# Kernel optimization log

Hardware: AMD Instinct MI355X
Metric: run time of the kernel (lower is better)

The kernel has to match this reference:

```python
import jax, jax.numpy as jnp
import numpy as np

D = 256
H = 8
DH = D // H
EPS = 1e-3  # keras LayerNormalization default epsilon


def sinusoidal_pe(length, dim):
    pos = jnp.arange(length, dtype=jnp.float32)[:, None]            # [L,1]
    i = jnp.arange(0, dim, 2, dtype=jnp.float32)[None, :]           # [1,D/2]
    angle = pos / jnp.power(10000.0, i / dim)                        # [L,D/2]
    pe = jnp.zeros((length, dim), dtype=jnp.float32)
    pe = pe.at[:, 0::2].set(jnp.sin(angle))
    pe = pe.at[:, 1::2].set(jnp.cos(angle))
    return pe


def rel_shift(x):
    # x: [B,H,L,L] -> Transformer-XL relative shift
    B, h, L1, L2 = x.shape
    x = jnp.pad(x, ((0, 0), (0, 0), (0, 0), (1, 0)))                 # [B,H,L,L+1]
    x = x.reshape(B, h, L2 + 1, L1)[:, :, 1:, :]                     # drop first row
    return x.reshape(B, h, L1, L2)


def setup_inputs() -> dict:
    key = jax.random.key(0)
    ks = jax.random.split(key, 16)
    s = 0.02
    inp = {
        "x": jax.random.normal(ks[0], (4, 2048, D), dtype=jnp.float32),
        "gamma": jnp.ones((D,), dtype=jnp.float32),
        "beta": jnp.zeros((D,), dtype=jnp.float32),
        "Wq": jax.random.normal(ks[1], (D, D), dtype=jnp.float32) * s,
        "bq": jnp.zeros((D,), dtype=jnp.float32),
        "Wk": jax.random.normal(ks[2], (D, D), dtype=jnp.float32) * s,
        "bk": jnp.zeros((D,), dtype=jnp.float32),
        "Wv": jax.random.normal(ks[3], (D, D), dtype=jnp.float32) * s,
        "bv": jnp.zeros((D,), dtype=jnp.float32),
        "Wp": jax.random.normal(ks[4], (D, D), dtype=jnp.float32) * s,  # pos proj, no bias
        "u_bias": jax.random.normal(ks[5], (H, DH), dtype=jnp.float32) * s,
        "v_bias": jax.random.normal(ks[6], (H, DH), dtype=jnp.float32) * s,
        "Wo": jax.random.normal(ks[7], (D, D), dtype=jnp.float32) * s,
        "bo": jnp.zeros((D,), dtype=jnp.float32),
    }
    return inp


def reference(x, gamma, beta, Wq, bq, Wk, bk, Wv, bv, Wp, u_bias, v_bias, Wo, bo):
    B, L, _ = x.shape
    # pre-LN (keras LayerNormalization over last axis)
    mu = jnp.mean(x, axis=-1, keepdims=True)
    var = jnp.mean(jnp.square(x - mu), axis=-1, keepdims=True)
    xn = (x - mu) * jax.lax.rsqrt(var + EPS) * gamma + beta

    pe = sinusoidal_pe(L, D)                                          # [L,D] (tiled over batch implicitly)

    q = (xn @ Wq + bq).reshape(B, L, H, DH)                           # [B,L,H,dh]
    k = (xn @ Wk + bk).reshape(B, L, H, DH)
    v = (xn @ Wv + bv).reshape(B, L, H, DH)
    p = (pe @ Wp).reshape(L, H, DH)                                   # [L,H,dh]

    # content and position scores (Transformer-XL biases u, v)
    content = jnp.einsum("bqhd,bkhd->bhqk", q + u_bias[None, None], k)
    pos = jnp.einsum("bqhd,khd->bhqk", q + v_bias[None, None], p)
    pos = rel_shift(pos)
    score = (content + pos) / jnp.sqrt(jnp.float32(D))

    attn = jax.nn.softmax(score, axis=-1)                             # dropout inactive (inference)
    ctx = jnp.einsum("bhqk,bkhd->bqhd", attn, v).reshape(B, L, D)
    out = ctx @ Wo + bo                                               # final dropout inactive
    return out
```

## Files before the change

kernel.cpp:

```cpp
#include <hip/hip_runtime.h>
#include <hip/hip_bf16.h>
#include <math.h>

#define L_SEQ 2048
#define NB 4
#define DMODEL 256
#define NH 8
#define DHEAD 32
#define NROW (NB*L_SEQ)

typedef __attribute__((ext_vector_type(8))) short short8;
typedef __attribute__((ext_vector_type(4))) float f32x4;

__device__ __forceinline__ float bf2f(short v) {
    union { unsigned u; float f; } x; x.u = ((unsigned)(unsigned short)v) << 16; return x.f;
}
__device__ __forceinline__ short f2bf(float f) {
    union { float f; unsigned u; } x; x.f = f;
    unsigned r = x.u + 0x7fff + ((x.u >> 16) & 1);
    return (short)(r >> 16);
}
__device__ __forceinline__ short8 zero8() {
    short8 z;
    #pragma unroll
    for (int i = 0; i < 8; ++i) z[i] = 0;
    return z;
}

__global__ __launch_bounds__(256)
void prep_kernel(const float* __restrict__ x, const float* __restrict__ gamma,
                 const float* __restrict__ beta, short* __restrict__ xnb,
                 short* __restrict__ peb,
                 const float* __restrict__ W0, const float* __restrict__ W1,
                 const float* __restrict__ W2, const float* __restrict__ W3,
                 const float* __restrict__ W4, short* __restrict__ WT,
                 short* __restrict__ pext) {
    const int bid = blockIdx.x;
    __shared__ float s[64][65];
    if (bid < 2048) {
        int lane = threadIdx.x & 63;
        int row  = bid*4 + (threadIdx.x >> 6);
        const float4 a = *(const float4*)(x + (size_t)row*DMODEL + lane*4);
        float sm  = a.x+a.y+a.z+a.w;
        float s2 = a.x*a.x+a.y*a.y+a.z*a.z+a.w*a.w;
        #pragma unroll
        for (int o = 32; o; o >>= 1) { sm += __shfl_xor(sm,o); s2 += __shfl_xor(s2,o); }
        float mu  = sm * (1.f/DMODEL);
        float var = s2 * (1.f/DMODEL) - mu*mu;
        float rst = rsqrtf(var + 1e-3f);
        const float4 g  = *(const float4*)(gamma + lane*4);
        const float4 bt = *(const float4*)(beta  + lane*4);
        short4 o;
        o.x = f2bf((a.x-mu)*rst*g.x + bt.x);
        o.y = f2bf((a.y-mu)*rst*g.y + bt.y);
        o.z = f2bf((a.z-mu)*rst*g.z + bt.z);
        o.w = f2bf((a.w-mu)*rst*g.w + bt.w);
        *(short4*)(xnb + (size_t)row*DMODEL + lane*4) = o;
    } else if (bid < 3072) {
        int idx = (bid-2048)*256 + threadIdx.x;
        int l = idx >> 7, m = idx & 127;
        double ang = (double)l * exp((double)m * (-9.210340371976184/128.0));
        unsigned sv = (unsigned)(unsigned short)f2bf((float)sin(ang));
        unsigned cv = (unsigned)(unsigned short)f2bf((float)cos(ang));
        *(unsigned*)(peb + l*DMODEL + 2*m) = sv | (cv << 16);
    } else if (bid < 3152) {
        const int r  = bid - 3072;
        const int z  = r >> 4, rr = r & 15;
        const float* W = (z==0)?W0:(z==1)?W1:(z==2)?W2:(z==3)?W3:W4;
        short* O = WT + (size_t)z*65536;
        const int k0 = (rr >> 2)*64, n0 = (rr & 3)*64;
        const int c = threadIdx.x & 63, r4 = threadIdx.x >> 6;
        #pragma unroll
        for (int i = 0; i < 16; ++i) {
            int rw = r4 + 4*i;
            s[c][rw] = W[(size_t)(k0+rw)*256 + n0 + c];
        }
        __syncthreads();
        #pragma unroll
        for (int i = 0; i < 16; ++i) {
            int rn = r4 + 4*i;
            O[(size_t)(n0+rn)*256 + k0 + c] = f2bf(s[rn][c]);
        }
    } else {
        if (threadIdx.x < 64) {
            short4 z4 = {0,0,0,0};
            *(short4*)(pext + (size_t)L_SEQ*DMODEL + threadIdx.x*4) = z4;
        }
    }
}

__global__ __launch_bounds__(256, 2)
void projmm_kernel(const short* __restrict__ xnb, const short* __restrict__ peb,
                   const short* __restrict__ WT,
                   const float* __restrict__ bq, const float* __restrict__ bk,
                   const float* __restrict__ bv,
                   short* __restrict__ q, short* __restrict__ kb,
                   short* __restrict__ vT, short* __restrict__ pext) {
    const int bid = blockIdx.x;
    int z, rb;
    if (bid < 384) { z = bid >> 7; rb = bid & 127; }
    else           { z = 3;        rb = bid - 384; }
    const short* A = (z == 3) ? peb : xnb;
    const short* W = WT + (size_t)z*65536;
    const int t = threadIdx.x;
    const int w = t >> 6, l = t & 63, lc = l & 15, lg = l >> 4;
    const int m0 = rb*64 + 16*w;

    short8 afr[8];
    #pragma unroll
    for (int ks = 0; ks < 8; ++ks)
        afr[ks] = *(const short8*)(A + (size_t)(m0+lc)*256 + ks*32 + lg*8);

    const f32x4 zf = {0.f,0.f,0.f,0.f};
    f32x4 acc[16];
    #pragma unroll
    for (int ct = 0; ct < 16; ++ct) acc[ct] = zf;

    #pragma unroll
    for (int ct = 0; ct < 16; ++ct) {
        #pragma unroll
        for (int ks = 0; ks < 8; ++ks) {
            const short8 bfr = *(const short8*)(W + (size_t)(ct*16+lc)*256 + ks*32 + lg*8);
            acc[ct] = __builtin_amdgcn_mfma_f32_16x16x32_bf16(afr[ks], bfr, acc[ct], 0, 0, 0);
        }
    }

    if (z == 2) {
        const int bb = m0 >> 11;
        const int l0 = (m0 & 2047) + 4*lg;
        #pragma unroll
        for (int ct = 0; ct < 16; ++ct) {
            const int cc = ct*16 + lc;
            const float bias = bv[cc];
            const int hh = cc >> 5, dd = cc & 31;
            short4 o;
            o.x = f2bf(acc[ct][0] + bias);
            o.y = f2bf(acc[ct][1] + bias);
            o.z = f2bf(acc[ct][2] + bias);
            o.w = f2bf(acc[ct][3] + bias);
            *(short4*)(vT + ((size_t)((bb*NH + hh)*DHEAD + dd))*L_SEQ + l0) = o;
        }
    } else if (z == 3) {
        #pragma unroll
        for (int ct = 0; ct < 16; ++ct) {
            const int cc = ct*16 + lc;
            #pragma unroll
            for (int r = 0; r < 4; ++r) {
                const int rr = m0 + 4*lg + r;
                const short v = f2bf(acc[ct][r]);
                pext[(size_t)rr*DMODEL + cc] = v;
                pext[(size_t)(rr + L_SEQ + 1)*DMODEL + cc] = v;
            }
        }
    } else {
        #pragma unroll
        for (int ct = 0; ct < 16; ++ct) {
            const int cc = ct*16 + lc;
            const float bias = (z == 0) ? bq[cc] : bk[cc];
            #pragma unroll
            for (int r = 0; r < 4; ++r) {
                const size_t idx = (size_t)(m0 + 4*lg + r)*DMODEL + cc;
                const short v = f2bf(acc[ct][r] + bias);
                if (z == 0) q[idx] = v;
                else        kb[idx] = v;
            }
        }
    }
}

__global__ __launch_bounds__(256, 2)
void outmm_kernel(const short* __restrict__ ctxb, const short* __restrict__ WTo,
                  const float* __restrict__ bo, float* __restrict__ out) {
    const int rb = blockIdx.x;
    const int t = threadIdx.x;
    const int w = t >> 6, l = t & 63, lc = l & 15, lg = l >> 4;
    const int m0 = rb*64 + 16*w;

    short8 afr[8];
    #pragma unroll
    for (int ks = 0; ks < 8; ++ks)
        afr[ks] = *(const short8*)(ctxb + (size_t)(m0+lc)*256 + ks*32 + lg*8);

    const f32x4 zf = {0.f,0.f,0.f,0.f};
    f32x4 acc[16];
    #pragma unroll
    for (int ct = 0; ct < 16; ++ct) acc[ct] = zf;

    #pragma unroll
    for (int ct = 0; ct < 16; ++ct) {
        #pragma unroll
        for (int ks = 0; ks < 8; ++ks) {
            const short8 bfr = *(const short8*)(WTo + (size_t)(ct*16+lc)*256 + ks*32 + lg*8);
            acc[ct] = __builtin_amdgcn_mfma_f32_16x16x32_bf16(afr[ks], bfr, acc[ct], 0, 0, 0);
        }
    }

    #pragma unroll
    for (int ct = 0; ct < 16; ++ct) {
        const int cc = ct*16 + lc;
        const float bias = bo[cc];
        #pragma unroll
        for (int r = 0; r < 4; ++r)
            out[(size_t)(m0 + 4*lg + r)*DMODEL + cc] = acc[ct][r] + bias;
    }
}

__global__ __launch_bounds__(256)
void attn_mfma_kernel(const short* __restrict__ qg, const short* __restrict__ kb,
                      const short* __restrict__ pext, const short* __restrict__ vT,
                      const float* __restrict__ ub, const float* __restrict__ vb,
                      short* __restrict__ ctxb) {
    const int i0  = blockIdx.x;
    const int xcd = i0 & 7, idx = i0 >> 3;
    const int h   = xcd;
    const int b   = idx >> 4;
    const int w   = threadIdx.x >> 6;
    const int q0  = (idx & 15) * 128 + 32 * w;
    const int l   = threadIdx.x & 63;
    const int lc  = l & 15;
    const int lg  = l >> 4;

    __shared__ float    sT[4][2][17][84];
    __shared__ unsigned sPk[4][2][2][16][32];

    const float KSC = 0.0625f * 1.44269504088896340736f;

    short8 aqu[2], aqv[2], aqv_sh[2];
    #pragma unroll
    for (int g = 0; g < 2; ++g) {
        const int r1 = q0 + 16*g + lc;
        const short8 qraw = *(const short8*)(qg + ((size_t)(b*L_SEQ + r1))*DMODEL + h*DHEAD + lg*8);
        short8 qraw_sh = zero8();
        if (r1 + 1 < L_SEQ)
            qraw_sh = *(const short8*)(qg + ((size_t)(b*L_SEQ + r1 + 1))*DMODEL + h*DHEAD + lg*8);
        #pragma unroll
        for (int j = 0; j < 8; ++j) {
            const float u_ = ub[h*DHEAD + lg*8 + j];
            const float v_ = vb[h*DHEAD + lg*8 + j];
            const float f  = bf2f(qraw[j]);
            aqu[g][j]    = f2bf((f + u_) * KSC);
            aqv[g][j]    = f2bf((f + v_) * KSC);
            aqv_sh[g][j] = f2bf((bf2f(qraw_sh[j]) + v_) * KSC);
        }
    }

    float m_r[2] = {-3.0e38f, -3.0e38f}, l_r[2] = {0.f, 0.f};
    f32x4 acc[2][2];
    #pragma unroll
    for (int g = 0; g < 2; ++g)
        #pragma unroll
        for (int dt = 0; dt < 2; ++dt)
            acc[g][dt] = (f32x4){0.f,0.f,0.f,0.f};
    const f32x4 zf = {0.f, 0.f, 0.f, 0.f};

    const short* kfetch = kb + ((size_t)(b*L_SEQ) + lc)*DMODEL + h*DHEAD + lg*8;
    const short* pcur   = pext + ((size_t)(L_SEQ - 32 - q0 + lc))*DMODEL + h*DHEAD + lg*8;
    const short* vcur   = vT + ((size_t)((b*NH + h)*DHEAD + lc))*L_SEQ + lg*8;

    short8 kfrag[4], pfrag[6], vfrag[2][2];
    #pragma unroll
    for (int ct = 0; ct < 4; ++ct)
        kfrag[ct] = *(const short8*)(kfetch + (size_t)ct*16*DMODEL);
    #pragma unroll
    for (int s = 0; s < 6; ++s)
        pfrag[s] = *(const short8*)(pcur + (size_t)s*16*DMODEL);
    kfetch += (size_t)64*DMODEL;

    const int colc = 4*lg + 15 - lc;
    const float* gb0[2] = { &sT[w][0][lc][colc],   &sT[w][1][lc][colc]   };
    const float* gb1[2] = { &sT[w][0][lc+1][colc], &sT[w][1][lc+1][colc] };
    const int swkey = lc & 7;

    for (int k0 = 0; k0 < L_SEQ; k0 += 64) {
        const int diff = k0 - q0;
        const int tbuf = (k0 >> 6) & 1;

        f32x4 cts[2][4];
        #pragma unroll
        for (int ct = 0; ct < 4; ++ct) {
            cts[0][ct] = __builtin_amdgcn_mfma_f32_16x16x32_bf16(kfrag[ct], aqu[0], zf, 0, 0, 0);
            cts[1][ct] = __builtin_amdgcn_mfma_f32_16x16x32_bf16(kfrag[ct], aqu[1], zf, 0, 0, 0);
        }

        #pragma unroll
        for (int g = 0; g < 2; ++g) {
            const int cthr = 17 - diff + 16*g;
            const int sb = 1 - g;
            if (cthr > 78) {
                #pragma unroll
                for (int cc = 0; cc < 5; ++cc) {
                    f32x4 tt = __builtin_amdgcn_mfma_f32_16x16x32_bf16(pfrag[cc+sb], aqv[g], zf, 0, 0, 0);
                    *(f32x4*)&sT[w][g][lc][16*cc + 4*lg] = tt;
                }
            } else if (cthr <= 0) {
                #pragma unroll
                for (int cc = 0; cc < 5; ++cc) {
                    f32x4 tt = __builtin_amdgcn_mfma_f32_16x16x32_bf16(pfrag[cc+sb], aqv_sh[g], zf, 0, 0, 0);
                    *(f32x4*)&sT[w][g][lc][16*cc + 4*lg] = tt;
                }
            } else {
                #pragma unroll
                for (int cc = 0; cc < 5; ++cc) {
                    f32x4 tt = __builtin_amdgcn_mfma_f32_16x16x32_bf16(pfrag[cc+sb], aqv[g], zf, 0, 0, 0);
                    *(f32x4*)&sT[w][g][lc][16*cc + 4*lg] = tt;
                    f32x4 tt2 = __builtin_amdgcn_mfma_f32_16x16x32_bf16(pfrag[cc+sb], aqv_sh[g], zf, 0, 0, 0);
                    if (lc == 15) *(f32x4*)&sT[w][g][16][16*cc + 4*lg] = tt2;
                }
            }
        }

        pfrag[0] = pfrag[4];
        pfrag[1] = pfrag[5];
        if (k0 + 64 < L_SEQ) {
            #pragma unroll
            for (int ct = 0; ct < 4; ++ct)
                kfrag[ct] = *(const short8*)(kfetch + (size_t)ct*16*DMODEL);
            #pragma unroll
            for (int s = 2; s < 6; ++s)
                pfrag[s] = *(const short8*)(pcur + (size_t)(64 + 16*s)*DMODEL);
        }
        kfetch += (size_t)64*DMODEL;
        pcur   += (size_t)64*DMODEL;

        asm volatile("s_waitcnt lgkmcnt(0)" ::: "memory");

        if (k0) {
            #pragma unroll
            for (int kc = 0; kc < 2; ++kc) {
                const int idx2 = ((4*kc + lg) ^ swkey) << 2;
                const short8 bp0 = *(const short8*)&sPk[w][0][tbuf ^ 1][lc][idx2];
                const short8 bp1 = *(const short8*)&sPk[w][1][tbuf ^ 1][lc][idx2];
                acc[0][0] = __builtin_amdgcn_mfma_f32_16x16x32_bf16(vfrag[0][kc], bp0, acc[0][0], 0, 0, 0);
                acc[0][1] = __builtin_amdgcn_mfma_f32_16x16x32_bf16(vfrag[1][kc], bp0, acc[0][1], 0, 0, 0);
                acc[1][0] = __builtin_amdgcn_mfma_f32_16x16x32_bf16(vfrag[0][kc], bp1, acc[1][0], 0, 0, 0);
                acc[1][1] = __builtin_amdgcn_mfma_f32_16x16x32_bf16(vfrag[1][kc], bp1, acc[1][1], 0, 0, 0);
            }
        }
        #pragma unroll
        for (int dt = 0; dt < 2; ++dt)
            #pragma unroll
            for (int kc = 0; kc < 2; ++kc)
                vfrag[dt][kc] = *(const short8*)(vcur + (size_t)dt*16*L_SEQ + kc*32);
        vcur += 64;

        float sc[2][4][4];
        float pmax[2];
        #pragma unroll
        for (int g = 0; g < 2; ++g) {
            const int cthr = 17 - diff + 16*g;
            if (cthr > 78 || cthr <= 0) {
                #pragma unroll
                for (int ct = 0; ct < 4; ++ct)
                    #pragma unroll
                    for (int r = 0; r < 4; ++r)
                        sc[g][ct][r] = cts[g][ct][r] + gb0[g][16*ct + r];
            } else {
                #pragma unroll
                for (int ct = 0; ct < 4; ++ct)
                    #pragma unroll
                    for (int r = 0; r < 4; ++r) {
                        const bool up = (16*ct + colc + r) >= cthr;
                        sc[g][ct][r] = cts[g][ct][r] + (up ? gb1[g] : gb0[g])[16*ct + r];
                    }
            }
            pmax[g] = sc[g][0][0];
            #pragma unroll
            for (int ct = 0; ct < 4; ++ct)
                #pragma unroll
                for (int r = 0; r < 4; ++r) pmax[g] = fmaxf(pmax[g], sc[g][ct][r]);
        }
        if (!__all(fmaxf(pmax[0] - m_r[0], pmax[1] - m_r[1]) <= 8.0f)) {
            #pragma unroll
            for (int g = 0; g < 2; ++g) {
                float mx = fmaxf(pmax[g], __shfl_xor(pmax[g], 16));
                mx = fmaxf(mx, __shfl_xor(mx, 32));
                const float mn = fmaxf(m_r[g], mx);
                const float alpha = exp2f(m_r[g] - mn);
                m_r[g] = mn;
                l_r[g] *= alpha;
                acc[g][0][0]*=alpha; acc[g][0][1]*=alpha; acc[g][0][2]*=alpha; acc[g][0][3]*=alpha;
                acc[g][1][0]*=alpha; acc[g][1][1]*=alpha; acc[g][1][2]*=alpha; acc[g][1][3]*=alpha;
            }
        }
        #pragma unroll
        for (int g = 0; g < 2; ++g) {
            float ts = 0.f;
            #pragma unroll
            for (int ct = 0; ct < 4; ++ct)
                #pragma unroll
                for (int r = 0; r < 4; ++r) {
                    sc[g][ct][r] = exp2f(sc[g][ct][r] - m_r[g]);
                    ts += sc[g][ct][r];
                }
            l_r[g] += ts;
            #pragma unroll
            for (int ct = 0; ct < 4; ++ct) {
                unsigned lo, hi;
                asm("v_cvt_pk_bf16_f32 %0, %1, %2" : "=v"(lo) : "v"(sc[g][ct][0]), "v"(sc[g][ct][1]));
                asm("v_cvt_pk_bf16_f32 %0, %1, %2" : "=v"(hi) : "v"(sc[g][ct][2]), "v"(sc[g][ct][3]));
                const int kbi = 2*ct + (lg >> 1);
                const int idx2 = ((kbi ^ swkey) << 2) + 2*(lg & 1);
                *(uint2*)&sPk[w][g][tbuf][lc][idx2] = make_uint2(lo, hi);
            }
        }
    }

    asm volatile("s_waitcnt lgkmcnt(0)" ::: "memory");
    #pragma unroll
    for (int kc = 0; kc < 2; ++kc) {
        const int idx2 = ((4*kc + lg) ^ swkey) << 2;
        const short8 bp0 = *(const short8*)&sPk[w][0][1][lc][idx2];
        const short8 bp1 = *(const short8*)&sPk[w][1][1][lc][idx2];
        acc[0][0] = __builtin_amdgcn_mfma_f32_16x16x32_bf16(vfrag[0][kc], bp0, acc[0][0], 0, 0, 0);
        acc[0][1] = __builtin_amdgcn_mfma_f32_16x16x32_bf16(vfrag[1][kc], bp0, acc[0][1], 0, 0, 0);
        acc[1][0] = __builtin_amdgcn_mfma_f32_16x16x32_bf16(vfrag[0][kc], bp1, acc[1][0], 0, 0, 0);
        acc[1][1] = __builtin_amdgcn_mfma_f32_16x16x32_bf16(vfrag[1][kc], bp1, acc[1][1], 0, 0, 0);
    }
    #pragma unroll
    for (int g = 0; g < 2; ++g) {
        float lr = l_r[g];
        lr += __shfl_xor(lr, 16);
        lr += __shfl_xor(lr, 32);
        float* sCt = (float*)&sPk[w][g][0][0][0];
        const float inv = 1.f / lr;
        f32x4 o0, o1;
        #pragma unroll
        for (int r = 0; r < 4; ++r) { o0[r] = acc[g][0][r]*inv; o1[r] = acc[g][1][r]*inv; }
        *(f32x4*)&sCt[lc*32 + 4*lg]      = o0;
        *(f32x4*)&sCt[lc*32 + 16 + 4*lg] = o1;
    }
    asm volatile("s_waitcnt lgkmcnt(0)" ::: "memory");
    #pragma unroll
    for (int g = 0; g < 2; ++g) {
        const float* sCt = (const float*)&sPk[w][g][0][0][0];
        const int rr = l >> 2;
        const int c0 = (l & 3) * 8;
        short8 ob;
        #pragma unroll
        for (int j = 0; j < 8; ++j) ob[j] = f2bf(sCt[rr*32 + c0 + j]);
        *(short8*)(ctxb + ((size_t)(b*L_SEQ + q0 + 16*g + rr))*DMODEL + h*DHEAD + c0) = ob;
    }
}

extern "C" void kernel_launch(void* const* d_in, const int* in_sizes, int n_in,
                              void* d_out, int out_size, void* d_ws, size_t ws_size,
                              hipStream_t stream) {
    (void)in_sizes; (void)n_in; (void)out_size; (void)ws_size;
    const float* x     = (const float*)d_in[0];
    const float* gamma = (const float*)d_in[1];
    const float* beta  = (const float*)d_in[2];
    const float* Wq    = (const float*)d_in[3];
    const float* bq    = (const float*)d_in[4];
    const float* Wk    = (const float*)d_in[5];
    const float* bk    = (const float*)d_in[6];
    const float* Wv    = (const float*)d_in[7];
    const float* bv    = (const float*)d_in[8];
    const float* Wp    = (const float*)d_in[9];
    const float* ub    = (const float*)d_in[10];
    const float* vb    = (const float*)d_in[11];
    const float* Wo    = (const float*)d_in[12];
    const float* bo    = (const float*)d_in[13];
    float* out = (float*)d_out;

    char* wsb = (char*)d_ws;
    short* ctxb = (short*)wsb;
    short* xnb  = (short*)(wsb + 4194304);
    short* peb  = (short*)(wsb + 4194304 + 4194304);
    short* WT   = (short*)(wsb + 4194304 + 4194304 + 1048576);
    short* q    = WT  + (size_t)5*65536;
    short* kbf  = q   + (size_t)NROW*DMODEL;
    short* vT   = kbf + (size_t)NROW*DMODEL;
    short* pext = vT  + (size_t)NROW*DMODEL;

    prep_kernel<<<3153, 256, 0, stream>>>(x, gamma, beta, xnb, peb,
                                          Wq, Wk, Wv, Wp, Wo, WT, pext);
    projmm_kernel<<<416, 256, 0, stream>>>(xnb, peb, WT, bq, bk, bv, q, kbf, vT, pext);
    attn_mfma_kernel<<<512, 256, 0, stream>>>(q, kbf, pext, vT, ub, vb, ctxb);
    outmm_kernel<<<128, 256, 0, stream>>>(ctxb, WT + (size_t)4*65536, bo, out);
}
```

Baseline: 160.3 us.

## Give each attention wave 64 query rows and halve block size to 128 threads

Each wave in the attention kernel now processes 64 query rows (four 16-row groups) instead of 32, and each block uses 2 waves instead of 4. The goal is to reuse each loaded K, P and V fragment across more query rows, which cuts global load traffic per row. K fragments for the next tile are now prefetched into separate registers, and the softmax is done per group instead of jointly. The PE table is also computed with float sinf/cosf/__expf instead of double precision, which lowers prep cost but may slightly change the PE values. The larger register footprint and fewer waves per block may reduce occupancy and latency hiding.

```diff
diff --git a/kernel.cpp b/kernel.cpp
--- a/kernel.cpp
+++ b/kernel.cpp
@@ -59,9 +59,9 @@
     } else if (bid < 3072) {
         int idx = (bid-2048)*256 + threadIdx.x;
         int l = idx >> 7, m = idx & 127;
-        double ang = (double)l * exp((double)m * (-9.210340371976184/128.0));
-        unsigned sv = (unsigned)(unsigned short)f2bf((float)sin(ang));
-        unsigned cv = (unsigned)(unsigned short)f2bf((float)cos(ang));
+        float ang = (float)l * __expf((float)m * (-9.210340371976184f/128.0f));
+        unsigned sv = (unsigned)(unsigned short)f2bf(sinf(ang));
+        unsigned cv = (unsigned)(unsigned short)f2bf(cosf(ang));
         *(unsigned*)(peb + l*DMODEL + 2*m) = sv | (cv << 16);
     } else if (bid < 3152) {
         const int r  = bid - 3072;
@@ -205,7 +205,7 @@
     }
 }
 
-__global__ __launch_bounds__(256)
+__global__ __launch_bounds__(128)
 void attn_mfma_kernel(const short* __restrict__ qg, const short* __restrict__ kb,
                       const short* __restrict__ pext, const short* __restrict__ vT,
                       const float* __restrict__ ub, const float* __restrict__ vb,
@@ -215,20 +215,20 @@
     const int h   = xcd;
     const int b   = idx >> 4;
     const int w   = threadIdx.x >> 6;
-    const int q0  = (idx & 15) * 128 + 32 * w;
+    const int qb  = (idx & 15) * 128 + 64 * w;
     const int l   = threadIdx.x & 63;
     const int lc  = l & 15;
     const int lg  = l >> 4;
 
-    __shared__ float    sT[4][2][17][84];
-    __shared__ unsigned sPk[4][2][2][16][32];
+    __shared__ float    sT[2][4][17][84];
+    __shared__ unsigned sPk[2][4][2][16][32];
 
     const float KSC = 0.0625f * 1.44269504088896340736f;
 
-    short8 aqu[2], aqv[2], aqv_sh[2];
-    #pragma unroll
-    for (int g = 0; g < 2; ++g) {
-        const int r1 = q0 + 16*g + lc;
+    short8 aqu[4], aqv[4], aqv_sh[4];
+    #pragma unroll
+    for (int g = 0; g < 4; ++g) {
+        const int r1 = qb + 16*g + lc;
         const short8 qraw = *(const short8*)(qg + ((size_t)(b*L_SEQ + r1))*DMODEL + h*DHEAD + lg*8);
         short8 qraw_sh = zero8();
         if (r1 + 1 < L_SEQ)
@@ -244,48 +244,40 @@
         }
     }
 
-    float m_r[2] = {-3.0e38f, -3.0e38f}, l_r[2] = {0.f, 0.f};
-    f32x4 acc[2][2];
-    #pragma unroll
-    for (int g = 0; g < 2; ++g)
-        #pragma unroll
-        for (int dt = 0; dt < 2; ++dt)
-            acc[g][dt] = (f32x4){0.f,0.f,0.f,0.f};
+    float m_r[4], l_r[4];
+    f32x4 acc[4][2];
+    #pragma unroll
+    for (int g = 0; g < 4; ++g) {
+        m_r[g] = -3.0e38f; l_r[g] = 0.f;
+        acc[g][0] = (f32x4){0.f,0.f,0.f,0.f};
+        acc[g][1] = (f32x4){0.f,0.f,0.f,0.f};
+    }
     const f32x4 zf = {0.f, 0.f, 0.f, 0.f};
 
     const short* kfetch = kb + ((size_t)(b*L_SEQ) + lc)*DMODEL + h*DHEAD + lg*8;
-    const short* pcur   = pext + ((size_t)(L_SEQ - 32 - q0 + lc))*DMODEL + h*DHEAD + lg*8;
+    const short* pcur   = pext + ((size_t)(L_SEQ - 64 - qb + lc))*DMODEL + h*DHEAD + lg*8;
     const short* vcur   = vT + ((size_t)((b*NH + h)*DHEAD + lc))*L_SEQ + lg*8;
 
-    short8 kfrag[4], pfrag[6], vfrag[2][2];
+    short8 kfrag[4], kfnxt[4], pfrag[8], vfrag[2][2];
     #pragma unroll
     for (int ct = 0; ct < 4; ++ct)
         kfrag[ct] = *(const short8*)(kfetch + (size_t)ct*16*DMODEL);
     #pragma unroll
-    for (int s = 0; s < 6; ++s)
+    for (int s = 0; s < 8; ++s)
         pfrag[s] = *(const short8*)(pcur + (size_t)s*16*DMODEL);
     kfetch += (size_t)64*DMODEL;
 
     const int colc = 4*lg + 15 - lc;
-    const float* gb0[2] = { &sT[w][0][lc][colc],   &sT[w][1][lc][colc]   };
-    const float* gb1[2] = { &sT[w][0][lc+1][colc], &sT[w][1][lc+1][colc] };
     const int swkey = lc & 7;
 
     for (int k0 = 0; k0 < L_SEQ; k0 += 64) {
-        const int diff = k0 - q0;
+        const int diff = k0 - qb;
         const int tbuf = (k0 >> 6) & 1;
 
-        f32x4 cts[2][4];
-        #pragma unroll
-        for (int ct = 0; ct < 4; ++ct) {
-            cts[0][ct] = __builtin_amdgcn_mfma_f32_16x16x32_bf16(kfrag[ct], aqu[0], zf, 0, 0, 0);
-            cts[1][ct] = __builtin_amdgcn_mfma_f32_16x16x32_bf16(kfrag[ct], aqu[1], zf, 0, 0, 0);
-        }
-
-        #pragma unroll
-        for (int g = 0; g < 2; ++g) {
+        #pragma unroll
+        for (int g = 0; g < 4; ++g) {
             const int cthr = 17 - diff + 16*g;
-            const int sb = 1 - g;
+            const int sb = 3 - g;
             if (cthr > 78) {
                 #pragma unroll
                 for (int cc = 0; cc < 5; ++cc) {
@@ -309,14 +301,14 @@
             }
         }
 
-        pfrag[0] = pfrag[4];
-        pfrag[1] = pfrag[5];
+        #pragma unroll
+        for (int s = 0; s < 4; ++s) pfrag[s] = pfrag[s+4];
         if (k0 + 64 < L_SEQ) {
             #pragma unroll
             for (int ct = 0; ct < 4; ++ct)
-                kfrag[ct] = *(const short8*)(kfetch + (size_t)ct*16*DMODEL);
-            #pragma unroll
-            for (int s = 2; s < 6; ++s)
+                kfnxt[ct] = *(const short8*)(kfetch + (size_t)ct*16*DMODEL);
+            #pragma unroll
+            for (int s = 4; s < 8; ++s)
                 pfrag[s] = *(const short8*)(pcur + (size_t)(64 + 16*s)*DMODEL);
         }
         kfetch += (size_t)64*DMODEL;
@@ -328,12 +320,12 @@
             #pragma unroll
             for (int kc = 0; kc < 2; ++kc) {
                 const int idx2 = ((4*kc + lg) ^ swkey) << 2;
-                const short8 bp0 = *(const short8*)&sPk[w][0][tbuf ^ 1][lc][idx2];
-                const short8 bp1 = *(const short8*)&sPk[w][1][tbuf ^ 1][lc][idx2];
-                acc[0][0] = __builtin_amdgcn_mfma_f32_16x16x32_bf16(vfrag[0][kc], bp0, acc[0][0], 0, 0, 0);
-                acc[0][1] = __builtin_amdgcn_mfma_f32_16x16x32_bf16(vfrag[1][kc], bp0, acc[0][1], 0, 0, 0);
-                acc[1][0] = __builtin_amdgcn_mfma_f32_16x16x32_bf16(vfrag[0][kc], bp1, acc[1][0], 0, 0, 0);
-                acc[1][1] = __builtin_amdgcn_mfma_f32_16x16x32_bf16(vfrag[1][kc], bp1, acc[1][1], 0, 0, 0);
+                #pragma unroll
+                for (int g = 0; g < 4; ++g) {
+                    const short8 bp = *(const short8*)&sPk[w][g][tbuf ^ 1][lc][idx2];
+                    acc[g][0] = __builtin_amdgcn_mfma_f32_16x16x32_bf16(vfrag[0][kc], bp, acc[g][0], 0, 0, 0);
+                    acc[g][1] = __builtin_amdgcn_mfma_f32_16x16x32_bf16(vfrag[1][kc], bp, acc[g][1], 0, 0, 0);
+                }
             }
         }
         #pragma unroll
@@ -343,81 +335,86 @@
                 vfrag[dt][kc] = *(const short8*)(vcur + (size_t)dt*16*L_SEQ + kc*32);
         vcur += 64;
 
-        float sc[2][4][4];
-        float pmax[2];
-        #pragma unroll
-        for (int g = 0; g < 2; ++g) {
+        #pragma unroll
+        for (int g = 0; g < 4; ++g) {
             const int cthr = 17 - diff + 16*g;
+            f32x4 cts[4];
+            #pragma unroll
+            for (int ct = 0; ct < 4; ++ct)
+                cts[ct] = __builtin_amdgcn_mfma_f32_16x16x32_bf16(kfrag[ct], aqu[g], zf, 0, 0, 0);
+
+            const float* gb0 = &sT[w][g][lc][colc];
+            const float* gb1 = &sT[w][g][lc+1][colc];
+            float sc[4][4];
             if (cthr > 78 || cthr <= 0) {
                 #pragma unroll
                 for (int ct = 0; ct < 4; ++ct)
                     #pragma unroll
                     for (int r = 0; r < 4; ++r)
-                        sc[g][ct][r] = cts[g][ct][r] + gb0[g][16*ct + r];
+                        sc[ct][r] = cts[ct][r] + gb0[16*ct + r];
             } else {
                 #pragma unroll
                 for (int ct = 0; ct < 4; ++ct)
                     #pragma unroll
                     for (int r = 0; r < 4; ++r) {
                         const bool up = (16*ct + colc + r) >= cthr;
-                        sc[g][ct][r] = cts[g][ct][r] + (up ? gb1[g] : gb0[g])[16*ct + r];
+                        sc[ct][r] = cts[ct][r] + (up ? gb1 : gb0)[16*ct + r];
                     }
             }
-            pmax[g] = sc[g][0][0];
+
+            float pmax = sc[0][0];
             #pragma unroll
             for (int ct = 0; ct < 4; ++ct)
                 #pragma unroll
-                for (int r = 0; r < 4; ++r) pmax[g] = fmaxf(pmax[g], sc[g][ct][r]);
-        }
-        if (!__all(fmaxf(pmax[0] - m_r[0], pmax[1] - m_r[1]) <= 8.0f)) {
-            #pragma unroll
-            for (int g = 0; g < 2; ++g) {
-                float mx = fmaxf(pmax[g], __shfl_xor(pmax[g], 16));
+                for (int r = 0; r < 4; ++r) pmax = fmaxf(pmax, sc[ct][r]);
+            if (!__all(pmax - m_r[g] <= 8.0f)) {
+                float mx = fmaxf(pmax, __shfl_xor(pmax, 16));
                 mx = fmaxf(mx, __shfl_xor(mx, 32));
                 const float mn = fmaxf(m_r[g], mx);
                 const float alpha = exp2f(m_r[g] - mn);
                 m_r[g] = mn;
                 l_r[g] *= alpha;
-                acc[g][0][0]*=alpha; acc[g][0][1]*=alpha; acc[g][0][2]*=alpha; acc[g][0][3]*=alpha;
-                acc[g][1][0]*=alpha; acc[g][1][1]*=alpha; acc[g][1][2]*=alpha; acc[g][1][3]*=alpha;
-            }
-        }
-        #pragma unroll
-        for (int g = 0; g < 2; ++g) {
+                #pragma unroll
+                for (int r = 0; r < 4; ++r) { acc[g][0][r] *= alpha; acc[g][1][r] *= alpha; }
+            }
             float ts = 0.f;
             #pragma unroll
             for (int ct = 0; ct < 4; ++ct)
                 #pragma unroll
                 for (int r = 0; r < 4; ++r) {
-                    sc[g][ct][r] = exp2f(sc[g][ct][r] - m_r[g]);
-                    ts += sc[g][ct][r];
+                    sc[ct][r] = exp2f(sc[ct][r] - m_r[g]);
+                    ts += sc[ct][r];
                 }
             l_r[g] += ts;
+
             #pragma unroll
             for (int ct = 0; ct < 4; ++ct) {
                 unsigned lo, hi;
-                asm("v_cvt_pk_bf16_f32 %0, %1, %2" : "=v"(lo) : "v"(sc[g][ct][0]), "v"(sc[g][ct][1]));
-                asm("v_cvt_pk_bf16_f32 %0, %1, %2" : "=v"(hi) : "v"(sc[g][ct][2]), "v"(sc[g][ct][3]));
+                asm("v_cvt_pk_bf16_f32 %0, %1, %2" : "=v"(lo) : "v"(sc[ct][0]), "v"(sc[ct][1]));
+                asm("v_cvt_pk_bf16_f32 %0, %1, %2" : "=v"(hi) : "v"(sc[ct][2]), "v"(sc[ct][3]));
                 const int kbi = 2*ct + (lg >> 1);
                 const int idx2 = ((kbi ^ swkey) << 2) + 2*(lg & 1);
                 *(uint2*)&sPk[w][g][tbuf][lc][idx2] = make_uint2(lo, hi);
             }
         }
+
+        #pragma unroll
+        for (int ct = 0; ct < 4; ++ct) kfrag[ct] = kfnxt[ct];
     }
 
     asm volatile("s_waitcnt lgkmcnt(0)" ::: "memory");
     #pragma unroll
     for (int kc = 0; kc < 2; ++kc) {
         const int idx2 = ((4*kc + lg) ^ swkey) << 2;
-        const short8 bp0 = *(const short8*)&sPk[w][0][1][lc][idx2];
-        const short8 bp1 = *(const short8*)&sPk[w][1][1][lc][idx2];
-        acc[0][0] = __builtin_amdgcn_mfma_f32_16x16x32_bf16(vfrag[0][kc], bp0, acc[0][0], 0, 0, 0);
-        acc[0][1] = __builtin_amdgcn_mfma_f32_16x16x32_bf16(vfrag[1][kc], bp0, acc[0][1], 0, 0, 0);
-        acc[1][0] = __builtin_amdgcn_mfma_f32_16x16x32_bf16(vfrag[0][kc], bp1, acc[1][0], 0, 0, 0);
-        acc[1][1] = __builtin_amdgcn_mfma_f32_16x16x32_bf16(vfrag[1][kc], bp1, acc[1][1], 0, 0, 0);
-    }
-    #pragma unroll
-    for (int g = 0; g < 2; ++g) {
+        #pragma unroll
+        for (int g = 0; g < 4; ++g) {
+            const short8 bp = *(const short8*)&sPk[w][g][1][lc][idx2];
+            acc[g][0] = __builtin_amdgcn_mfma_f32_16x16x32_bf16(vfrag[0][kc], bp, acc[g][0], 0, 0, 0);
+            acc[g][1] = __builtin_amdgcn_mfma_f32_16x16x32_bf16(vfrag[1][kc], bp, acc[g][1], 0, 0, 0);
+        }
+    }
+    #pragma unroll
+    for (int g = 0; g < 4; ++g) {
         float lr = l_r[g];
         lr += __shfl_xor(lr, 16);
         lr += __shfl_xor(lr, 32);
@@ -431,14 +428,14 @@
     }
     asm volatile("s_waitcnt lgkmcnt(0)" ::: "memory");
     #pragma unroll
-    for (int g = 0; g < 2; ++g) {
+    for (int g = 0; g < 4; ++g) {
         const float* sCt = (const float*)&sPk[w][g][0][0][0];
         const int rr = l >> 2;
         const int c0 = (l & 3) * 8;
         short8 ob;
         #pragma unroll
         for (int j = 0; j < 8; ++j) ob[j] = f2bf(sCt[rr*32 + c0 + j]);
-        *(short8*)(ctxb + ((size_t)(b*L_SEQ + q0 + 16*g + rr))*DMODEL + h*DHEAD + c0) = ob;
+        *(short8*)(ctxb + ((size_t)(b*L_SEQ + qb + 16*g + rr))*DMODEL + h*DHEAD + c0) = ob;
     }
 }
 
@@ -475,6 +472,6 @@
     prep_kernel<<<3153, 256, 0, stream>>>(x, gamma, beta, xnb, peb,
                                           Wq, Wk, Wv, Wp, Wo, WT, pext);
     projmm_kernel<<<416, 256, 0, stream>>>(xnb, peb, WT, bq, bk, bv, q, kbf, vT, pext);
-    attn_mfma_kernel<<<512, 256, 0, stream>>>(q, kbf, pext, vT, ub, vb, ctxb);
+    attn_mfma_kernel<<<512, 128, 0, stream>>>(q, kbf, pext, vT, ub, vb, ctxb);
     outmm_kernel<<<128, 256, 0, stream>>>(ctxb, WT + (size_t)4*65536, bo, out);
 }
```

Result: slower. 198.9 us, median of 2 (+24.1%).
